# Kernel tuning notes

Measured on AMD Instinct MI355X. Metric: run time of the kernel, lower is better.

The kernel has to match this reference:

```python
import jax, jax.numpy as jnp
import numpy as np

EMBED_DIM = 1024
NUM_HEADS = 16
HEAD_DIM = EMBED_DIM // NUM_HEADS
B, S = 4, 2048


def setup_inputs() -> dict:
    key = jax.random.key(0)
    ks = jax.random.split(key, 9)
    scale = 1.0 / np.sqrt(EMBED_DIM)
    x = jax.random.normal(ks[0], (B, S, EMBED_DIM), dtype=jnp.float32)
    Wq = jax.random.uniform(ks[1], (EMBED_DIM, EMBED_DIM), jnp.float32, -scale, scale)
    bq = jax.random.uniform(ks[2], (EMBED_DIM,), jnp.float32, -scale, scale)
    Wk = jax.random.uniform(ks[3], (EMBED_DIM, EMBED_DIM), jnp.float32, -scale, scale)
    bk = jax.random.uniform(ks[4], (EMBED_DIM,), jnp.float32, -scale, scale)
    Wv = jax.random.uniform(ks[5], (EMBED_DIM, EMBED_DIM), jnp.float32, -scale, scale)
    bv = jax.random.uniform(ks[6], (EMBED_DIM,), jnp.float32, -scale, scale)
    Wo = jax.random.uniform(ks[7], (EMBED_DIM, EMBED_DIM), jnp.float32, -scale, scale)
    bo = jax.random.uniform(ks[8], (EMBED_DIM,), jnp.float32, -scale, scale)
    return {"x": x, "Wq": Wq, "bq": bq, "Wk": Wk, "bk": bk, "Wv": Wv, "bv": bv, "Wo": Wo, "bo": bo}


def reference(x, Wq, bq, Wk, bk, Wv, bv, Wo, bo):
    b, s, d = x.shape
    h, hd = NUM_HEADS, HEAD_DIM
    # projections -> [b, h, s, hd]
    def proj(W, bias):
        return (x @ W + bias).reshape(b, s, h, hd).transpose(0, 2, 1, 3)
    q = proj(Wq, bq)
    k = proj(Wk, bk)
    v = proj(Wv, bv)
    logits = jnp.einsum('bhqd,bhkd->bhqk', q, k) / np.sqrt(hd).astype(np.float32)
    attn = jax.nn.softmax(logits, axis=-1)  # dropout p=0.0 -> identity
    vals = jnp.einsum('bhqk,bhkd->bhqd', attn, v)
    vals = vals.transpose(0, 2, 1, 3).reshape(b, s, d)
    return vals @ Wo + bo
```

## Files before the change

kernel.cpp:

```cpp
#include <hip/hip_runtime.h>

typedef unsigned short u16;
typedef unsigned int u32;
typedef __bf16 bf16x8 __attribute__((ext_vector_type(8)));
typedef float f32x4 __attribute__((ext_vector_type(4)));
typedef float f32x16 __attribute__((ext_vector_type(16)));
typedef u32 u32x4 __attribute__((ext_vector_type(4)));
typedef u32 u32x2 __attribute__((ext_vector_type(2)));

#define NBATCH 4
#define NS 2048
#define ND 1024
#define NH 16
#define HDIM 64

#define MFMA(a, b, c) __builtin_amdgcn_mfma_f32_16x16x32_bf16(a, b, c, 0, 0, 0)
#define MFMA32(a, b, c) __builtin_amdgcn_mfma_f32_32x32x16_bf16(a, b, c, 0, 0, 0)

__device__ __forceinline__ u16 f2bf(float f) {
    u32 u = __builtin_bit_cast(u32, f);
    u += 0x7fffu + ((u >> 16) & 1u);
    return (u16)(u >> 16);
}

__device__ __forceinline__ u32 cvtpk(float a, float b) {
    u32 r;
    asm("v_cvt_pk_bf16_f32 %0, %1, %2" : "=v"(r) : "v"(a), "v"(b));
    return r;
}

__device__ __forceinline__ bf16x8 ldfrag(const u16* p) {
    u32x4 v = *(const u32x4*)p;
    return __builtin_bit_cast(bf16x8, v);
}

__device__ __forceinline__ void gld16(u16* lds, const u16* g) {
    __builtin_amdgcn_global_load_lds((__attribute__((address_space(1))) u32*)g,
                                     (__attribute__((address_space(3))) u32*)lds, 16, 0, 0);
}

__global__ __launch_bounds__(256) void cvt_f32_bf16(const float* __restrict__ src,
                                                    u16* __restrict__ dst) {
    const size_t i = ((size_t)blockIdx.x * 256 + threadIdx.x) * 4;
    float4 v = *(const float4*)(src + i);
    uint2 o;
    o.x = (u32)f2bf(v.x) | ((u32)f2bf(v.y) << 16);
    o.y = (u32)f2bf(v.z) | ((u32)f2bf(v.w) << 16);
    *(uint2*)(dst + i) = o;
}

__global__ __launch_bounds__(256) void wtrans(const float* __restrict__ W, u16* __restrict__ WT) {
    __shared__ u16 t[64][72];
    const int tid = threadIdx.x;
    const int k0 = blockIdx.x * 64, n0 = blockIdx.y * 64;
    {
        const int r = tid >> 2, cq = (tid & 3) * 16;
#pragma unroll
        for (int i = 0; i < 4; ++i) {
            float4 v = *(const float4*)(W + (size_t)(k0 + r) * ND + n0 + cq + i * 4);
            t[r][cq + i * 4 + 0] = f2bf(v.x);
            t[r][cq + i * 4 + 1] = f2bf(v.y);
            t[r][cq + i * 4 + 2] = f2bf(v.z);
            t[r][cq + i * 4 + 3] = f2bf(v.w);
        }
    }
    __syncthreads();
    {
        const int rr = tid >> 2, cq = (tid & 3) * 16;
        u32x4 o0, o1;
#pragma unroll
        for (int j = 0; j < 4; ++j) {
            o0[j] = (u32)t[cq + 2 * j][rr] | ((u32)t[cq + 2 * j + 1][rr] << 16);
            o1[j] = (u32)t[cq + 8 + 2 * j][rr] | ((u32)t[cq + 8 + 2 * j + 1][rr] << 16);
        }
        u16* out = WT + (size_t)(n0 + rr) * ND + k0 + cq;
        *(u32x4*)out = o0;
        *(u32x4*)(out + 8) = o1;
    }
}

template <int MODE>
__global__ __launch_bounds__(256) void gemm_bt(const u16* __restrict__ A, const u16* __restrict__ Bt,
                                               const float* __restrict__ bias, u16* __restrict__ obf,
                                               float* __restrict__ of32, float scale) {
    __shared__ u16 la[128 * 32];
    __shared__ u16 lb[128 * 32];
    const int tid = threadIdx.x;
    const int l = tid & 63, w = tid >> 6;
    const int lr = l & 15, lg = l >> 4;
    const int wr = w >> 1, wc = w & 1;
    const int m0 = blockIdx.y * 128, n0 = blockIdx.x * 128;

    const int idx0 = tid, idx1 = tid + 256;
    const int row0 = idx0 >> 2, row1 = idx1 >> 2;
    const int sc0 = ((idx0 & 3) ^ ((row0 >> 1) & 3)) * 8;
    const int sc1 = ((idx1 & 3) ^ ((row1 >> 1) & 3)) * 8;
    const u16* Ar0 = A + (size_t)(m0 + row0) * ND + sc0;
    const u16* Ar1 = A + (size_t)(m0 + row1) * ND + sc1;
    const u16* Br0 = Bt + (size_t)(n0 + row0) * ND + sc0;
    const u16* Br1 = Bt + (size_t)(n0 + row1) * ND + sc1;

    f32x4 acc[4][4] = {};

    for (int kt = 0; kt < 32; ++kt) {
        const int k0 = kt * 32;
        __syncthreads();
        gld16(&la[idx0 * 8], Ar0 + k0);
        gld16(&la[idx1 * 8], Ar1 + k0);
        gld16(&lb[idx0 * 8], Br0 + k0);
        gld16(&lb[idx1 * 8], Br1 + k0);
        __syncthreads();

        bf16x8 af[4], bv[4];
#pragma unroll
        for (int mb = 0; mb < 4; ++mb) {
            int row = wr * 64 + mb * 16 + lr;
            int off = row * 32 + (((lg * 16) ^ (((row >> 1) & 3) << 4)) >> 1);
            af[mb] = ldfrag(&la[off]);
        }
#pragma unroll
        for (int nb = 0; nb < 4; ++nb) {
            int row = wc * 64 + nb * 16 + lr;
            int off = row * 32 + (((lg * 16) ^ (((row >> 1) & 3) << 4)) >> 1);
            bv[nb] = ldfrag(&lb[off]);
        }
#pragma unroll
        for (int mb = 0; mb < 4; ++mb)
#pragma unroll
            for (int nb = 0; nb < 4; ++nb)
                acc[mb][nb] = MFMA(af[mb], bv[nb], acc[mb][nb]);
    }

#pragma unroll
    for (int mb = 0; mb < 4; ++mb) {
#pragma unroll
        for (int nb = 0; nb < 4; ++nb) {
            const int col = n0 + wc * 64 + nb * 16 + lr;
            const float bia = bias[col];
            if (MODE == 5) {
                const int hd = col & 63, h = col >> 6;
                const int rowb = m0 + wr * 64 + mb * 16 + lg * 4;
                const int b = rowb >> 11, kv = rowb & 2047;
                const int bh = b * NH + h;
                const int kt = kv >> 6, ks = (kv >> 4) & 3, hif = (kv >> 3) & 1, j0 = kv & 7;
                const int lane = (hd & 31) | (hif << 5);
                u32x2 o;
                o[0] = (u32)f2bf(acc[mb][nb][0] + bia) | ((u32)f2bf(acc[mb][nb][1] + bia) << 16);
                o[1] = (u32)f2bf(acc[mb][nb][2] + bia) | ((u32)f2bf(acc[mb][nb][3] + bia) << 16);
                size_t off = (size_t)bh * 131072 + (size_t)kt * 4096 +
                             (size_t)(((ks + 4 * (hd >> 5)) * 64 + lane) * 8 + j0);
                *(u32x2*)(obf + off) = o;
            } else {
#pragma unroll
                for (int r = 0; r < 4; ++r) {
                    const int rowg = m0 + wr * 64 + mb * 16 + lg * 4 + r;
                    float v = (acc[mb][nb][r] + bia) * scale;
                    if (MODE == 2) {
                        of32[(size_t)rowg * ND + col] = v;
                    } else if (MODE == 4) {
                        const int hd = col & 63, h = col >> 6;
                        const int b = rowg >> 11, kv = rowg & 2047;
                        const int bh = b * NH + h;
                        const int kt = kv >> 6, kvb = (kv >> 5) & 1;
                        const int lane = (kv & 31) | (((hd >> 3) & 1) << 5);
                        size_t o = (size_t)bh * 131072 + (size_t)kt * 4096 +
                                   (size_t)(((kvb * 4 + (hd >> 4)) * 64 + lane) * 8 + (hd & 7));
                        obf[o] = f2bf(v);
                    } else {
                        size_t o = ((size_t)((rowg >> 11) * NH + (col >> 6)) * NS + (rowg & 2047)) * HDIM + (col & 63);
                        obf[o] = f2bf(v);
                    }
                }
            }
        }
    }
}

__global__ __launch_bounds__(256) void attn(const u16* __restrict__ Q, const u16* __restrict__ Kf,
                                            const u16* __restrict__ Vf, u16* __restrict__ AO) {
    __shared__ u16 sm[16384];
    const int tid = threadIdx.x;
    const int l = tid & 63, w = tid >> 6;
    const int lq = l & 31, hi = l >> 5;
    const int qb = blockIdx.x, bh = blockIdx.y;
    const int qbase = qb * 128 + w * 32;

    const u16* Qrow = Q + ((size_t)bh * NS + qbase + lq) * HDIM;
    bf16x8 qf[4];
#pragma unroll
    for (int kh = 0; kh < 4; ++kh) qf[kh] = ldfrag(Qrow + kh * 16 + hi * 8);

    f32x16 oacc[2] = {};
    float ls0 = 0.f, ls1 = 0.f, ls2 = 0.f, ls3 = 0.f;

    const u16* KfB = Kf + (size_t)bh * 131072;
    const u16* VfB = Vf + (size_t)bh * 131072;

    gld16(sm + tid * 8, KfB + tid * 8);
    gld16(sm + (256 + tid) * 8, KfB + (256 + tid) * 8);
    gld16(sm + 8192 + tid * 8, VfB + tid * 8);
    gld16(sm + 8192 + (256 + tid) * 8, VfB + (256 + tid) * 8);
    __syncthreads();

    for (int kt = 0; kt < 32; ++kt) {
        const int cur = kt & 1;
        if (kt < 31) {
            const u16* kg = KfB + (size_t)(kt + 1) * 4096;
            const u16* vg = VfB + (size_t)(kt + 1) * 4096;
            u16* kd = sm + (cur ^ 1) * 4096;
            u16* vd = sm + 8192 + (cur ^ 1) * 4096;
            gld16(kd + tid * 8, kg + tid * 8);
            gld16(kd + (256 + tid) * 8, kg + (256 + tid) * 8);
            gld16(vd + tid * 8, vg + tid * 8);
            gld16(vd + (256 + tid) * 8, vg + (256 + tid) * 8);
        }
        const u16* klb = sm + cur * 4096;
        const u16* vlb = sm + 8192 + cur * 4096;

        bf16x8 kf[2][4];
#pragma unroll
        for (int kvb = 0; kvb < 2; ++kvb)
#pragma unroll
            for (int kh = 0; kh < 4; ++kh)
                kf[kvb][kh] = ldfrag(klb + ((kvb * 4 + kh) * 64 + l) * 8);

        f32x16 sacc[2] = {};
        __builtin_amdgcn_s_setprio(1);
#pragma unroll
        for (int kvb = 0; kvb < 2; ++kvb)
#pragma unroll
            for (int kh = 0; kh < 4; ++kh)
                sacc[kvb] = MFMA32(kf[kvb][kh], qf[kh], sacc[kvb]);
        __builtin_amdgcn_s_setprio(0);

        bf16x8 vf[2][4];
#pragma unroll
        for (int hdb = 0; hdb < 2; ++hdb)
#pragma unroll
            for (int ks = 0; ks < 4; ++ks)
                vf[hdb][ks] = ldfrag(vlb + ((hdb * 4 + ks) * 64 + l) * 8);

#pragma unroll
        for (int kvb = 0; kvb < 2; ++kvb) {
#pragma unroll
            for (int i = 0; i < 16; i += 4) {
                float p0 = __builtin_amdgcn_exp2f(sacc[kvb][i + 0]);
                float p1 = __builtin_amdgcn_exp2f(sacc[kvb][i + 1]);
                float p2 = __builtin_amdgcn_exp2f(sacc[kvb][i + 2]);
                float p3 = __builtin_amdgcn_exp2f(sacc[kvb][i + 3]);
                sacc[kvb][i + 0] = p0;
                sacc[kvb][i + 1] = p1;
                sacc[kvb][i + 2] = p2;
                sacc[kvb][i + 3] = p3;
                ls0 += p0;
                ls1 += p1;
                ls2 += p2;
                ls3 += p3;
            }
        }

        bf16x8 pf[4];
#pragma unroll
        for (int ks = 0; ks < 4; ++ks) {
            const int i0 = 2 * ks, i1 = 2 * ks + 1;
            const int q20 = i0 & 3, kvb0 = i0 >> 2;
            const int q21 = i1 & 3, kvb1 = i1 >> 2;
            u32 W00 = cvtpk(sacc[kvb0][4 * q20 + 0], sacc[kvb0][4 * q20 + 1]);
            u32 W01 = cvtpk(sacc[kvb0][4 * q20 + 2], sacc[kvb0][4 * q20 + 3]);
            u32 W10 = cvtpk(sacc[kvb1][4 * q21 + 0], sacc[kvb1][4 * q21 + 1]);
            u32 W11 = cvtpk(sacc[kvb1][4 * q21 + 2], sacc[kvb1][4 * q21 + 3]);
            u32x2 s0 = __builtin_amdgcn_permlane32_swap(W00, W10, false, false);
            u32x2 s1 = __builtin_amdgcn_permlane32_swap(W01, W11, false, false);
            u32x4 words;
            words[0] = s0[0];
            words[1] = s1[0];
            words[2] = s0[1];
            words[3] = s1[1];
            pf[ks] = __builtin_bit_cast(bf16x8, words);
        }

        __builtin_amdgcn_s_setprio(1);
#pragma unroll
        for (int hdb = 0; hdb < 2; ++hdb)
#pragma unroll
            for (int ks = 0; ks < 4; ++ks)
                oacc[hdb] = MFMA32(vf[hdb][ks], pf[ks], oacc[hdb]);
        __builtin_amdgcn_s_setprio(0);

        __syncthreads();
    }

    float lsum = (ls0 + ls1) + (ls2 + ls3);
    lsum += __shfl_xor(lsum, 32);

    u16* ot = sm + w * 2048;
    const float inv = 1.f / lsum;
#pragma unroll
    for (int hdb = 0; hdb < 2; ++hdb)
#pragma unroll
        for (int q2 = 0; q2 < 4; ++q2)
#pragma unroll
            for (int rp = 0; rp < 2; ++rp) {
                u32 word = cvtpk(oacc[hdb][4 * q2 + 2 * rp] * inv, oacc[hdb][4 * q2 + 2 * rp + 1] * inv);
                const int hd0 = hdb * 32 + 8 * q2 + 4 * hi + 2 * rp;
                const int byteoff = lq * 128 + ((2 * hd0) ^ ((lq & 7) << 4));
                *(u32*)((char*)ot + byteoff) = word;
            }
    const int b = bh >> 4, h = bh & 15;
#pragma unroll
    for (int p = 0; p < 4; ++p) {
        const int idx = p * 64 + l;
        const int row = idx >> 3;
        const int cb = ((idx & 7) * 16) ^ ((row & 7) << 4);
        u32x4 val = *(u32x4*)((char*)ot + row * 128 + cb);
        *(u32x4*)(AO + ((size_t)b * NS + qbase + row) * ND + h * 64 + (idx & 7) * 8) = val;
    }
}

extern "C" void kernel_launch(void* const* d_in, const int* in_sizes, int n_in,
                              void* d_out, int out_size, void* d_ws, size_t ws_size,
                              hipStream_t stream) {
    const float* x = (const float*)d_in[0];
    const float* Wq = (const float*)d_in[1];
    const float* bq = (const float*)d_in[2];
    const float* Wk = (const float*)d_in[3];
    const float* bk = (const float*)d_in[4];
    const float* Wv = (const float*)d_in[5];
    const float* bv = (const float*)d_in[6];
    const float* Wo = (const float*)d_in[7];
    const float* bo = (const float*)d_in[8];
    float* out = (float*)d_out;

    u16* ws = (u16*)d_ws;
    u16* xb = ws;
    u16* wqT = ws + 8388608;
    u16* wkT = wqT + 1048576;
    u16* wvT = wkT + 1048576;
    u16* woT = wvT + 1048576;
    u16* Qp = woT + 1048576;
    u16* Kfp = Qp + 8388608;
    u16* Vfp = Kfp + 8388608;
    u16* AO = xb;

    cvt_f32_bf16<<<8192, 256, 0, stream>>>(x, xb);
    dim3 tg(16, 16);
    wtrans<<<tg, 256, 0, stream>>>(Wq, wqT);
    wtrans<<<tg, 256, 0, stream>>>(Wk, wkT);
    wtrans<<<tg, 256, 0, stream>>>(Wv, wvT);
    wtrans<<<tg, 256, 0, stream>>>(Wo, woT);
    dim3 gg(8, 64);
    gemm_bt<1><<<gg, 256, 0, stream>>>(xb, wqT, bq, Qp, nullptr, 1.0f);
    gemm_bt<4><<<gg, 256, 0, stream>>>(xb, wkT, bk, Kfp, nullptr, 0.125f * 1.44269504f);
    gemm_bt<5><<<gg, 256, 0, stream>>>(xb, wvT, bv, Vfp, nullptr, 1.0f);
    attn<<<dim3(16, 64), 256, 0, stream>>>(Qp, Kfp, Vfp, AO);
    gemm_bt<2><<<gg, 256, 0, stream>>>(AO, woT, bo, nullptr, out, 1.0f);
}
```

Measured before the change: 227.0 us.

## Merge QKV GEMMs into one launch and remap blocks for XCD locality

Replaces the three separate Q/K/V projection launches with a single 1536-block kernel that picks its weight, bias and output layout per region. The attention and output GEMM kernels use a 1D grid whose block index is remapped so that blocks landing on the same XCD share the same rows of x or the same batch-head. This is meant to cut launch overhead, fill the GPU in one wave set, and improve L2 reuse of A tiles and K/V within each XCD. It adds runtime branching on region in the epilogue and relies on round-robin block-to-XCD dispatch.

```diff
diff --git a/kernel.cpp b/kernel.cpp
--- a/kernel.cpp
+++ b/kernel.cpp
@@ -13,6 +13,7 @@
 #define ND 1024
 #define NH 16
 #define HDIM 64
+#define KSCALE (0.125f * 1.44269504f)
 
 #define MFMA(a, b, c) __builtin_amdgcn_mfma_f32_16x16x32_bf16(a, b, c, 0, 0, 0)
 #define MFMA32(a, b, c) __builtin_amdgcn_mfma_f32_32x32x16_bf16(a, b, c, 0, 0, 0)
@@ -79,17 +80,28 @@
     }
 }
 
-template <int MODE>
-__global__ __launch_bounds__(256) void gemm_bt(const u16* __restrict__ A, const u16* __restrict__ Bt,
-                                               const float* __restrict__ bias, u16* __restrict__ obf,
-                                               float* __restrict__ of32, float scale) {
+__global__ __launch_bounds__(256) void gemm_qkv(const u16* __restrict__ A,
+                                                const u16* __restrict__ wqT, const u16* __restrict__ wkT,
+                                                const u16* __restrict__ wvT,
+                                                const float* __restrict__ bq, const float* __restrict__ bk,
+                                                const float* __restrict__ bv,
+                                                u16* __restrict__ Qp, u16* __restrict__ Kf,
+                                                u16* __restrict__ Vf) {
     __shared__ u16 la[128 * 32];
     __shared__ u16 lb[128 * 32];
+    const int wg = blockIdx.x;
+    const int xcd = wg & 7, idx = wg >> 3;
+    const int ybl = xcd * 8 + idx / 24;
+    const int xbl = idx % 24;
+    const int region = xbl >> 3;
+    const int m0 = ybl * 128, n0 = (xbl & 7) * 128;
+    const u16* Bt = region == 0 ? wqT : region == 1 ? wkT : wvT;
+    const float* bias = region == 0 ? bq : region == 1 ? bk : bv;
+
     const int tid = threadIdx.x;
     const int l = tid & 63, w = tid >> 6;
     const int lr = l & 15, lg = l >> 4;
     const int wr = w >> 1, wc = w & 1;
-    const int m0 = blockIdx.y * 128, n0 = blockIdx.x * 128;
 
     const int idx0 = tid, idx1 = tid + 256;
     const int row0 = idx0 >> 2, row1 = idx1 >> 2;
@@ -111,7 +123,7 @@
         gld16(&lb[idx1 * 8], Br1 + k0);
         __syncthreads();
 
-        bf16x8 af[4], bv[4];
+        bf16x8 af[4], bv4[4];
 #pragma unroll
         for (int mb = 0; mb < 4; ++mb) {
             int row = wr * 64 + mb * 16 + lr;
@@ -122,13 +134,13 @@
         for (int nb = 0; nb < 4; ++nb) {
             int row = wc * 64 + nb * 16 + lr;
             int off = row * 32 + (((lg * 16) ^ (((row >> 1) & 3) << 4)) >> 1);
-            bv[nb] = ldfrag(&lb[off]);
+            bv4[nb] = ldfrag(&lb[off]);
         }
 #pragma unroll
         for (int mb = 0; mb < 4; ++mb)
 #pragma unroll
             for (int nb = 0; nb < 4; ++nb)
-                acc[mb][nb] = MFMA(af[mb], bv[nb], acc[mb][nb]);
+                acc[mb][nb] = MFMA(af[mb], bv4[nb], acc[mb][nb]);
     }
 
 #pragma unroll
@@ -137,40 +149,110 @@
         for (int nb = 0; nb < 4; ++nb) {
             const int col = n0 + wc * 64 + nb * 16 + lr;
             const float bia = bias[col];
-            if (MODE == 5) {
-                const int hd = col & 63, h = col >> 6;
+            const int hd = col & 63, h = col >> 6;
+            if (region == 2) {
                 const int rowb = m0 + wr * 64 + mb * 16 + lg * 4;
                 const int b = rowb >> 11, kv = rowb & 2047;
                 const int bh = b * NH + h;
-                const int kt = kv >> 6, ks = (kv >> 4) & 3, hif = (kv >> 3) & 1, j0 = kv & 7;
+                const int ktp = kv >> 6, ks = (kv >> 4) & 3, hif = (kv >> 3) & 1, j0 = kv & 7;
                 const int lane = (hd & 31) | (hif << 5);
                 u32x2 o;
                 o[0] = (u32)f2bf(acc[mb][nb][0] + bia) | ((u32)f2bf(acc[mb][nb][1] + bia) << 16);
                 o[1] = (u32)f2bf(acc[mb][nb][2] + bia) | ((u32)f2bf(acc[mb][nb][3] + bia) << 16);
-                size_t off = (size_t)bh * 131072 + (size_t)kt * 4096 +
+                size_t off = (size_t)bh * 131072 + (size_t)ktp * 4096 +
                              (size_t)(((ks + 4 * (hd >> 5)) * 64 + lane) * 8 + j0);
-                *(u32x2*)(obf + off) = o;
-            } else {
+                *(u32x2*)(Vf + off) = o;
+            } else if (region == 1) {
 #pragma unroll
                 for (int r = 0; r < 4; ++r) {
                     const int rowg = m0 + wr * 64 + mb * 16 + lg * 4 + r;
-                    float v = (acc[mb][nb][r] + bia) * scale;
-                    if (MODE == 2) {
-                        of32[(size_t)rowg * ND + col] = v;
-                    } else if (MODE == 4) {
-                        const int hd = col & 63, h = col >> 6;
-                        const int b = rowg >> 11, kv = rowg & 2047;
-                        const int bh = b * NH + h;
-                        const int kt = kv >> 6, kvb = (kv >> 5) & 1;
-                        const int lane = (kv & 31) | (((hd >> 3) & 1) << 5);
-                        size_t o = (size_t)bh * 131072 + (size_t)kt * 4096 +
-                                   (size_t)(((kvb * 4 + (hd >> 4)) * 64 + lane) * 8 + (hd & 7));
-                        obf[o] = f2bf(v);
-                    } else {
-                        size_t o = ((size_t)((rowg >> 11) * NH + (col >> 6)) * NS + (rowg & 2047)) * HDIM + (col & 63);
-                        obf[o] = f2bf(v);
-                    }
+                    float v = (acc[mb][nb][r] + bia) * KSCALE;
+                    const int b = rowg >> 11, kv = rowg & 2047;
+                    const int bh = b * NH + h;
+                    const int ktp = kv >> 6, kvb = (kv >> 5) & 1;
+                    const int lane = (kv & 31) | (((hd >> 3) & 1) << 5);
+                    size_t o = (size_t)bh * 131072 + (size_t)ktp * 4096 +
+                               (size_t)(((kvb * 4 + (hd >> 4)) * 64 + lane) * 8 + (hd & 7));
+                    Kf[o] = f2bf(v);
                 }
+            } else {
+#pragma unroll
+                for (int r = 0; r < 4; ++r) {
+                    const int rowg = m0 + wr * 64 + mb * 16 + lg * 4 + r;
+                    float v = acc[mb][nb][r] + bia;
+                    size_t o = ((size_t)((rowg >> 11) * NH + h) * NS + (rowg & 2047)) * HDIM + hd;
+                    Qp[o] = f2bf(v);
+                }
+            }
+        }
+    }
+}
+
+__global__ __launch_bounds__(256) void gemm_o(const u16* __restrict__ A, const u16* __restrict__ Bt,
+                                              const float* __restrict__ bias, float* __restrict__ of32) {
+    __shared__ u16 la[128 * 32];
+    __shared__ u16 lb[128 * 32];
+    const int wg = blockIdx.x;
+    const int xcd = wg & 7, idx = wg >> 3;
+    const int ybl = xcd * 8 + (idx >> 3);
+    const int xbl = idx & 7;
+    const int m0 = ybl * 128, n0 = xbl * 128;
+
+    const int tid = threadIdx.x;
+    const int l = tid & 63, w = tid >> 6;
+    const int lr = l & 15, lg = l >> 4;
+    const int wr = w >> 1, wc = w & 1;
+
+    const int idx0 = tid, idx1 = tid + 256;
+    const int row0 = idx0 >> 2, row1 = idx1 >> 2;
+    const int sc0 = ((idx0 & 3) ^ ((row0 >> 1) & 3)) * 8;
+    const int sc1 = ((idx1 & 3) ^ ((row1 >> 1) & 3)) * 8;
+    const u16* Ar0 = A + (size_t)(m0 + row0) * ND + sc0;
+    const u16* Ar1 = A + (size_t)(m0 + row1) * ND + sc1;
+    const u16* Br0 = Bt + (size_t)(n0 + row0) * ND + sc0;
+    const u16* Br1 = Bt + (size_t)(n0 + row1) * ND + sc1;
+
+    f32x4 acc[4][4] = {};
+
+    for (int kt = 0; kt < 32; ++kt) {
+        const int k0 = kt * 32;
+        __syncthreads();
+        gld16(&la[idx0 * 8], Ar0 + k0);
+        gld16(&la[idx1 * 8], Ar1 + k0);
+        gld16(&lb[idx0 * 8], Br0 + k0);
+        gld16(&lb[idx1 * 8], Br1 + k0);
+        __syncthreads();
+
+        bf16x8 af[4], bv4[4];
+#pragma unroll
+        for (int mb = 0; mb < 4; ++mb) {
+            int row = wr * 64 + mb * 16 + lr;
+            int off = row * 32 + (((lg * 16) ^ (((row >> 1) & 3) << 4)) >> 1);
+            af[mb] = ldfrag(&la[off]);
+        }
+#pragma unroll
+        for (int nb = 0; nb < 4; ++nb) {
+            int row = wc * 64 + nb * 16 + lr;
+            int off = row * 32 + (((lg * 16) ^ (((row >> 1) & 3) << 4)) >> 1);
+            bv4[nb] = ldfrag(&lb[off]);
+        }
+#pragma unroll
+        for (int mb = 0; mb < 4; ++mb)
+#pragma unroll
+            for (int nb = 0; nb < 4; ++nb)
+                acc[mb][nb] = MFMA(af[mb], bv4[nb], acc[mb][nb]);
+    }
+
+#pragma unroll
+    for (int mb = 0; mb < 4; ++mb) {
+#pragma unroll
+        for (int nb = 0; nb < 4; ++nb) {
+            const int col = n0 + wc * 64 + nb * 16 + lr;
+            const float bia = bias[col];
+#pragma unroll
+            for (int r = 0; r < 4; ++r) {
+                const int rowg = m0 + wr * 64 + mb * 16 + lg * 4 + r;
+                of32[(size_t)rowg * ND + col] = acc[mb][nb][r] + bia;
             }
         }
     }
@@ -182,7 +264,10 @@
     const int tid = threadIdx.x;
     const int l = tid & 63, w = tid >> 6;
     const int lq = l & 31, hi = l >> 5;
-    const int qb = blockIdx.x, bh = blockIdx.y;
+    const int wg = blockIdx.x;
+    const int xcd = wg & 7, idx = wg >> 3;
+    const int bh = xcd * 8 + (idx >> 4);
+    const int qb = idx & 15;
     const int qbase = qb * 128 + w * 32;
 
     const u16* Qrow = Q + ((size_t)bh * NS + qbase + lq) * HDIM;
@@ -309,11 +394,11 @@
     const int b = bh >> 4, h = bh & 15;
 #pragma unroll
     for (int p = 0; p < 4; ++p) {
-        const int idx = p * 64 + l;
-        const int row = idx >> 3;
-        const int cb = ((idx & 7) * 16) ^ ((row & 7) << 4);
+        const int pidx = p * 64 + l;
+        const int row = pidx >> 3;
+        const int cb = ((pidx & 7) * 16) ^ ((row & 7) << 4);
         u32x4 val = *(u32x4*)((char*)ot + row * 128 + cb);
-        *(u32x4*)(AO + ((size_t)b * NS + qbase + row) * ND + h * 64 + (idx & 7) * 8) = val;
+        *(u32x4*)(AO + ((size_t)b * NS + qbase - w * 32 + w * 32 + row) * ND + h * 64 + (pidx & 7) * 8) = val;
     }
 }
 
@@ -348,10 +433,7 @@
     wtrans<<<tg, 256, 0, stream>>>(Wk, wkT);
     wtrans<<<tg, 256, 0, stream>>>(Wv, wvT);
     wtrans<<<tg, 256, 0, stream>>>(Wo, woT);
-    dim3 gg(8, 64);
-    gemm_bt<1><<<gg, 256, 0, stream>>>(xb, wqT, bq, Qp, nullptr, 1.0f);
-    gemm_bt<4><<<gg, 256, 0, stream>>>(xb, wkT, bk, Kfp, nullptr, 0.125f * 1.44269504f);
-    gemm_bt<5><<<gg, 256, 0, stream>>>(xb, wvT, bv, Vfp, nullptr, 1.0f);
-    attn<<<dim3(16, 64), 256, 0, stream>>>(Qp, Kfp, Vfp, AO);
-    gemm_bt<2><<<gg, 256, 0, stream>>>(AO, woT, bo, nullptr, out, 1.0f);
-}
+    gemm_qkv<<<1536, 256, 0, stream>>>(xb, wqT, wkT, wvT, bq, bk, bv, Qp, Kfp, Vfp);
+    attn<<<1024, 256, 0, stream>>>(Qp, Kfp, Vfp, AO);
+    gemm_o<<<512, 256, 0, stream>>>(AO, woT, bo, out);
+}
```

New measurement: 214.7 us. -5.4%, faster.
